# Performance work log

Hardware: AMD Instinct MI355X
Metric: run time of the kernel (lower is better)

Reference implementation:

```python
import jax, jax.numpy as jnp
import numpy as np

NEG_INF = -1e9
LEAKY_SLOPE = 0.2


def setup_inputs() -> dict:
    key = jax.random.key(0)
    k1, k2, k3, k4, k5, k6, k7 = jax.random.split(key, 7)
    B, L = 50000, 50          # batch nodes, max padded neighbors (num_sample)
    N = 200000                # unique node embeddings
    D_in, D_out = 256, 64
    padded_neighs = jax.random.randint(k1, (B, L), 0, N, dtype=jnp.int32)
    mask = jax.random.randint(k2, (B, L), 0, 2, dtype=jnp.int32).astype(jnp.bool_)
    mask = mask.at[:, 0].set(True)  # every node has >=1 neighbor
    dst_idx = jax.random.randint(k3, (B,), 0, N, dtype=jnp.int32)
    embed_table = jax.random.normal(k4, (N, D_in), dtype=jnp.float32)
    # xavier_uniform for proj [D_out, D_in]
    bound = float(np.sqrt(6.0 / (D_in + D_out)))
    W_proj = jax.random.uniform(k5, (D_out, D_in), minval=-bound, maxval=bound, dtype=jnp.float32)
    a_src = jax.random.normal(k6, (D_out,), dtype=jnp.float32) * 0.1
    a_dst = jax.random.normal(k7, (D_out,), dtype=jnp.float32) * 0.1
    return {"padded_neighs": padded_neighs, "mask": mask, "dst_idx": dst_idx,
            "embed_table": embed_table, "W_proj": W_proj, "a_src": a_src, "a_dst": a_dst}


def leaky_relu(x):
    return jnp.where(x >= 0, x, LEAKY_SLOPE * x)


def reference(padded_neighs, mask, dst_idx, embed_table, W_proj, a_src, a_dst):
    # project all unique-node embeddings: [N, D_out]
    embed_prime = embed_table @ W_proj.T
    # gather neighbor and dst projected features
    neigh_feats = embed_prime[padded_neighs]          # [B, L, D_out]
    dst_feats = embed_prime[dst_idx]                  # [B, D_out] (constant across L)
    # GAT-style scores: leaky_relu(dst @ a_dst) + leaky_relu(neigh @ a_src)
    dst_attn = leaky_relu(dst_feats @ a_dst)[:, None, None]       # [B, 1, 1]
    neigh_attn = leaky_relu(neigh_feats @ a_src)[:, :, None]      # [B, L, 1]
    edge_attn = dst_attn + neigh_attn                             # [B, L, 1]
    # masked softmax over the neighbor axis
    scores = jnp.where(mask[:, :, None], edge_attn, NEG_INF)
    attn = jax.nn.softmax(scores, axis=1)                         # [B, L, 1]
    # weighted sum of neighbor features
    return jnp.sum(attn * neigh_feats, axis=1)                    # [B, D_out]
```

## Files before the change

### kernel.cpp

```cpp
#include <hip/hip_runtime.h>
#include <stdint.h>

#define DIN 256
#define DOUT 64
#define LMAX 50
#define NEG_INF -1e9f
#define WSTRIDE 264

typedef short bf16x8 __attribute__((ext_vector_type(8)));
typedef float f32x4  __attribute__((ext_vector_type(4)));

static __device__ __forceinline__ unsigned short f2bf(float x) {
    unsigned int u = __float_as_uint(x);
    u += 0x7fffu + ((u >> 16) & 1u);
    return (unsigned short)(u >> 16);
}
static __device__ __forceinline__ float bflo(unsigned int u) { return __uint_as_float(u << 16); }
static __device__ __forceinline__ float bfhi(unsigned int u) { return __uint_as_float(u & 0xffff0000u); }

__global__ __launch_bounds__(256) void proj_kernel(
    const float* __restrict__ embed, const float* __restrict__ W,
    unsigned short* __restrict__ ep16, int N)
{
    __shared__ unsigned short wl[64 * WSTRIDE];

    const int tid  = threadIdx.x;
    const int lane = tid & 63;
    const int wv   = tid >> 6;
    const int mrow = lane & 15;
    const int quad = lane >> 4;

#pragma unroll
    for (int i = 0; i < 16; ++i) {
        const int idx4 = tid + 256 * i;
        const int e    = idx4 * 4;
        const int n    = e >> 8;
        const int k    = e & 255;
        const float4 f = *(const float4*)&W[e];
        union { unsigned short s[4]; unsigned long long v; } p;
        p.s[0] = f2bf(f.x); p.s[1] = f2bf(f.y);
        p.s[2] = f2bf(f.z); p.s[3] = f2bf(f.w);
        *(unsigned long long*)&wl[n * WSTRIDE + k] = p.v;
    }
    __syncthreads();

    const int m_base = blockIdx.x * 128 + wv * 32;

    f32x4 acc[2][4];
#pragma unroll
    for (int mt = 0; mt < 2; ++mt)
#pragma unroll
        for (int nt = 0; nt < 4; ++nt) acc[mt][nt] = (f32x4){0.f, 0.f, 0.f, 0.f};

    for (int kc = 0; kc < DIN; kc += 32) {
        bf16x8 afrag[2];
#pragma unroll
        for (int mt = 0; mt < 2; ++mt) {
            int row = m_base + mt * 16 + mrow;
            if (row >= N) row = N - 1;
            const float* ap = embed + (size_t)row * DIN + kc + quad * 8;
            const float4 f0 = *(const float4*)ap;
            const float4 f1 = *(const float4*)(ap + 4);
            union { short s[8]; bf16x8 f; } a;
            a.s[0] = (short)f2bf(f0.x); a.s[1] = (short)f2bf(f0.y);
            a.s[2] = (short)f2bf(f0.z); a.s[3] = (short)f2bf(f0.w);
            a.s[4] = (short)f2bf(f1.x); a.s[5] = (short)f2bf(f1.y);
            a.s[6] = (short)f2bf(f1.z); a.s[7] = (short)f2bf(f1.w);
            afrag[mt] = a.f;
        }
#pragma unroll
        for (int nt = 0; nt < 4; ++nt) {
            const bf16x8 bfrag =
                *(const bf16x8*)&wl[(nt * 16 + mrow) * WSTRIDE + kc + quad * 8];
            acc[0][nt] = __builtin_amdgcn_mfma_f32_16x16x32_bf16(
                afrag[0], bfrag, acc[0][nt], 0, 0, 0);
            acc[1][nt] = __builtin_amdgcn_mfma_f32_16x16x32_bf16(
                afrag[1], bfrag, acc[1][nt], 0, 0, 0);
        }
    }

#pragma unroll
    for (int mt = 0; mt < 2; ++mt)
#pragma unroll
        for (int nt = 0; nt < 4; ++nt)
#pragma unroll
            for (int r = 0; r < 4; ++r) {
                const int row = m_base + mt * 16 + quad * 4 + r;
                if (row < N)
                    ep16[(size_t)row * DOUT + nt * 16 + mrow] = f2bf(acc[mt][nt][r]);
            }
}

__global__ __launch_bounds__(256, 6) void agg_kernel(
    const int* __restrict__ neighs, const void* __restrict__ mask,
    const int* __restrict__ dst_idx, const unsigned int* __restrict__ ep16u,
    const float* __restrict__ a_src, const float* __restrict__ a_dst,
    float* __restrict__ out, int B)
{
    __shared__ unsigned int fwbuf[4][LMAX * 32];
    __shared__ float attn_s[4][64];

    const int tid  = threadIdx.x;
    const int lane = tid & 63;
    const int wv   = tid >> 6;
    const int b    = blockIdx.x * 4 + wv;
    const int bc   = b < B ? b : B - 1;
    const int c    = lane & 31;

    const unsigned int* mw = (const unsigned int*)mask;
    const bool byteMode = (mw[12] > 1u);

    bool mvalid = false;
    if (lane < LMAX) {
        const int mi = bc * LMAX + lane;
        mvalid = byteMode ? (((const uint8_t*)mask)[mi] != 0)
                          : (((const int*)mask)[mi] != 0);
    }
    const unsigned long long vm = __ballot(mvalid);

    const int* nb = neighs + (size_t)bc * LMAX;
    const int n0  = nb[0];

    const unsigned int du = ep16u[(size_t)dst_idx[bc] * 32 + c];
    const float2 adv = *(const float2*)&a_dst[2 * c];

    unsigned int* buf = fwbuf[wv];
    const int gchunk = (lane & 7) ^ (lane >> 3);
#pragma unroll
    for (int i = 0; i < 6; ++i) {
        const int r = 8 * i + (lane >> 3);
        const int n = ((vm >> r) & 1ull) ? nb[r] : n0;
        const unsigned int* gp = ep16u + (size_t)n * 32 + gchunk * 4;
        __builtin_amdgcn_global_load_lds(
            (const __attribute__((address_space(1))) void*)gp,
            (__attribute__((address_space(3))) void*)&buf[i * 256],
            16, 0, 0);
    }
    {
        const int r   = 48 + (lane >> 5);
        const int n   = ((vm >> r) & 1ull) ? nb[r] : n0;
        const int w   = lane & 31;
        const int gwd = (((w >> 2) ^ (r & 7)) << 2) + (w & 3);
        const unsigned int* gp = ep16u + (size_t)n * 32 + gwd;
        __builtin_amdgcn_global_load_lds(
            (const __attribute__((address_space(1))) void*)gp,
            (__attribute__((address_space(3))) void*)&buf[48 * 32],
            4, 0, 0);
    }

    float pd = bflo(du) * adv.x + bfhi(du) * adv.y;
#pragma unroll
    for (int m = 32; m >= 1; m >>= 1) pd += __shfl_xor(pd, m, 64);
    pd *= 0.5f;
    const float dst_attn = pd >= 0.f ? pd : 0.2f * pd;

    __syncthreads();

    const int l    = lane < LMAX ? lane : 0;
    const int rot7 = l & 7;
    const unsigned int* fr = buf + l * 32;
    float dot = 0.f;
#pragma unroll
    for (int k8 = 0; k8 < 8; ++k8) {
        const uint4 u = *(const uint4*)&fr[((k8 ^ rot7) << 2)];
        dot = fmaf(bflo(u.x), a_src[k8 * 8 + 0], dot);
        dot = fmaf(bfhi(u.x), a_src[k8 * 8 + 1], dot);
        dot = fmaf(bflo(u.y), a_src[k8 * 8 + 2], dot);
        dot = fmaf(bfhi(u.y), a_src[k8 * 8 + 3], dot);
        dot = fmaf(bflo(u.z), a_src[k8 * 8 + 4], dot);
        dot = fmaf(bfhi(u.z), a_src[k8 * 8 + 5], dot);
        dot = fmaf(bflo(u.w), a_src[k8 * 8 + 6], dot);
        dot = fmaf(bfhi(u.w), a_src[k8 * 8 + 7], dot);
    }
    const float lr = dot >= 0.f ? dot : 0.2f * dot;
    float s = (lane < LMAX && mvalid) ? (dst_attn + lr) : NEG_INF;

    float mx = s;
#pragma unroll
    for (int m = 32; m >= 1; m >>= 1) mx = fmaxf(mx, __shfl_xor(mx, m, 64));
    const float e = __expf(s - mx);
    float se = e;
#pragma unroll
    for (int m = 32; m >= 1; m >>= 1) se += __shfl_xor(se, m, 64);
    attn_s[wv][lane] = e / se;

    const int half = lane >> 5;
    float acc0 = 0.f, acc1 = 0.f;
#pragma unroll
    for (int i = 0; i < 25; ++i) {
        const int r  = 2 * i + half;
        const int sw = (((c >> 2) ^ (r & 7)) << 2) + (c & 3);
        const unsigned int u = buf[r * 32 + sw];
        const float w = attn_s[wv][r];
        acc0 = fmaf(w, bflo(u), acc0);
        acc1 = fmaf(w, bfhi(u), acc1);
    }
    acc0 += __shfl_xor(acc0, 32, 64);
    acc1 += __shfl_xor(acc1, 32, 64);
    if (b < B && lane < 32) {
        float2 o; o.x = acc0; o.y = acc1;
        *(float2*)&out[(size_t)b * DOUT + 2 * c] = o;
    }
}

extern "C" void kernel_launch(void* const* d_in, const int* in_sizes, int n_in,
                              void* d_out, int out_size, void* d_ws, size_t ws_size,
                              hipStream_t stream)
{
    const int*   neighs  = (const int*)d_in[0];
    const void*  mask    = d_in[1];
    const int*   dst_idx = (const int*)d_in[2];
    const float* embed   = (const float*)d_in[3];
    const float* W       = (const float*)d_in[4];
    const float* a_src   = (const float*)d_in[5];
    const float* a_dst   = (const float*)d_in[6];
    float* out = (float*)d_out;

    const int B = in_sizes[2];
    const int N = in_sizes[3] / DIN;

    unsigned short* ep16 = (unsigned short*)d_ws;

    proj_kernel<<<dim3((N + 127) / 128), dim3(256), 0, stream>>>(embed, W, ep16, N);
    agg_kernel<<<dim3((B + 3) / 4), dim3(256), 0, stream>>>(
        neighs, mask, dst_idx, (const unsigned int*)ep16, a_src, a_dst, out, B);
}
```

Baseline: 377.7 us.

## Compact valid neighbors and gather only masked-in rows in aggregation

Uses ballot and popcount to compact the indices of valid neighbors into shared memory, then issues LDS-direct gathers only for those rows instead of all 50 padded slots. Dot, softmax and weighted-sum loops now run over the compacted count with dynamic trip counts. The block-wide __syncthreads is replaced by a per-wave vmcnt wait, since each wave uses only its own buffer. This cuts roughly half of the random global gather traffic under the random mask, at the cost of dynamic loops and a reliance on compiler-barrier asm for ordering of shared-memory accesses.

```diff
diff --git a/kernel.cpp b/kernel.cpp
--- a/kernel.cpp
+++ b/kernel.cpp
@@ -98,7 +98,7 @@
     float* __restrict__ out, int B)
 {
     __shared__ unsigned int fwbuf[4][LMAX * 32];
-    __shared__ float attn_s[4][64];
+    __shared__ unsigned int attn_s[4][64];
 
     const int tid  = threadIdx.x;
     const int lane = tid & 63;
@@ -117,34 +117,46 @@
                           : (((const int*)mask)[mi] != 0);
     }
     const unsigned long long vm = __ballot(mvalid);
+    const int nv = (int)__popcll(vm);
 
     const int* nb = neighs + (size_t)bc * LMAX;
-    const int n0  = nb[0];
+
+    unsigned int* cidx = attn_s[wv];
+    if (mvalid) {
+        const int p = (int)__popcll(vm & ((1ull << lane) - 1ull));
+        cidx[p] = (unsigned int)nb[lane];
+    }
+    asm volatile("" ::: "memory");
 
     const unsigned int du = ep16u[(size_t)dst_idx[bc] * 32 + c];
     const float2 adv = *(const float2*)&a_dst[2 * c];
 
     unsigned int* buf = fwbuf[wv];
-    const int gchunk = (lane & 7) ^ (lane >> 3);
-#pragma unroll
-    for (int i = 0; i < 6; ++i) {
-        const int r = 8 * i + (lane >> 3);
-        const int n = ((vm >> r) & 1ull) ? nb[r] : n0;
+    const int sub    = lane >> 3;
+    const int gchunk = (lane & 7) ^ sub;
+    const int f      = nv >> 3;
+    for (int i = 0; i < f; ++i) {
+        const int r = 8 * i + sub;
+        const int n = (int)cidx[r];
         const unsigned int* gp = ep16u + (size_t)n * 32 + gchunk * 4;
         __builtin_amdgcn_global_load_lds(
             (const __attribute__((address_space(1))) void*)gp,
             (__attribute__((address_space(3))) void*)&buf[i * 256],
             16, 0, 0);
     }
-    {
-        const int r   = 48 + (lane >> 5);
-        const int n   = ((vm >> r) & 1ull) ? nb[r] : n0;
+    const int t     = nv & 7;
+    const int npair = (t + 1) >> 1;
+    const int rbase = 8 * f;
+    for (int p2 = 0; p2 < npair; ++p2) {
+        const int r   = rbase + 2 * p2 + (lane >> 5);
+        const int rc  = r < nv ? r : nv - 1;
+        const int n   = (int)cidx[rc];
         const int w   = lane & 31;
         const int gwd = (((w >> 2) ^ (r & 7)) << 2) + (w & 3);
         const unsigned int* gp = ep16u + (size_t)n * 32 + gwd;
         __builtin_amdgcn_global_load_lds(
             (const __attribute__((address_space(1))) void*)gp,
-            (__attribute__((address_space(3))) void*)&buf[48 * 32],
+            (__attribute__((address_space(3))) void*)&buf[(rbase + 2 * p2) * 32],
             4, 0, 0);
     }
 
@@ -154,11 +166,11 @@
     pd *= 0.5f;
     const float dst_attn = pd >= 0.f ? pd : 0.2f * pd;
 
-    __syncthreads();
-
-    const int l    = lane < LMAX ? lane : 0;
-    const int rot7 = l & 7;
-    const unsigned int* fr = buf + l * 32;
+    asm volatile("s_waitcnt vmcnt(0)" ::: "memory");
+
+    const int lc   = lane < nv ? lane : nv - 1;
+    const int rot7 = lc & 7;
+    const unsigned int* fr = buf + lc * 32;
     float dot = 0.f;
 #pragma unroll
     for (int k8 = 0; k8 < 8; ++k8) {
@@ -173,7 +185,7 @@
         dot = fmaf(bfhi(u.w), a_src[k8 * 8 + 7], dot);
     }
     const float lr = dot >= 0.f ? dot : 0.2f * dot;
-    float s = (lane < LMAX && mvalid) ? (dst_attn + lr) : NEG_INF;
+    float s = (lane < nv) ? (dst_attn + lr) : NEG_INF;
 
     float mx = s;
 #pragma unroll
@@ -182,16 +194,18 @@
     float se = e;
 #pragma unroll
     for (int m = 32; m >= 1; m >>= 1) se += __shfl_xor(se, m, 64);
-    attn_s[wv][lane] = e / se;
+    attn_s[wv][lane] = __float_as_uint(e / se);
+    asm volatile("" ::: "memory");
 
     const int half = lane >> 5;
+    const int nit  = (nv + 1) >> 1;
     float acc0 = 0.f, acc1 = 0.f;
-#pragma unroll
-    for (int i = 0; i < 25; ++i) {
+    for (int i = 0; i < nit; ++i) {
         const int r  = 2 * i + half;
-        const int sw = (((c >> 2) ^ (r & 7)) << 2) + (c & 3);
-        const unsigned int u = buf[r * 32 + sw];
-        const float w = attn_s[wv][r];
+        const int rr = r < nv ? r : nv - 1;
+        const int sw = (((c >> 2) ^ (rr & 7)) << 2) + (c & 3);
+        const unsigned int u = buf[rr * 32 + sw];
+        const float w = __uint_as_float(attn_s[wv][r]);
         acc0 = fmaf(w, bflo(u), acc0);
         acc1 = fmaf(w, bfhi(u), acc1);
     }
```

Result: faster. 360.9 us (-4.5%).
